# Performance work log

Measured on AMD Instinct MI355X. Metric: run time of the kernel, lower is better.

Reference implementation:

```python
import jax, jax.numpy as jnp
import numpy as np
from jax import lax

IN_PLANES = 64
OUT_PLANES = 128
NSAMPLE = 16
BN_EPS = 1e-5


def setup_inputs() -> dict:
    key = jax.random.key(0)
    k1, k2, k3 = jax.random.split(key, 3)
    B, N = 8, 8192
    xyz = jax.random.normal(k1, (B, N, 3), jnp.float32)
    feature = jax.random.normal(k2, (B, N, IN_PLANES), jnp.float32)
    W = jax.random.normal(k3, (OUT_PLANES, IN_PLANES), jnp.float32) * (1.0 / np.sqrt(IN_PLANES))
    gamma = jnp.ones((OUT_PLANES,), jnp.float32)
    beta = jnp.zeros((OUT_PLANES,), jnp.float32)
    return {"xyz": xyz, "feature": feature, "W": W, "gamma": gamma, "beta": beta, "npoint": 2048}


def farthest_point_sample(xyz, npoint):
    # xyz: [B, N, 3] -> centroids: [B, npoint] int32. Deterministic start at index 0
    # (torch version uses a random start; math is otherwise identical).
    B, N, _ = xyz.shape

    def step(carry, _):
        distance, farthest = carry  # [B,N], [B]
        centroid = jnp.take_along_axis(xyz, farthest[:, None, None], axis=1)  # [B,1,3]
        dist = jnp.sum((xyz - centroid) ** 2, axis=-1)  # [B,N]
        distance = jnp.minimum(distance, dist)
        new_far = jnp.argmax(distance, axis=-1).astype(jnp.int32)
        return (distance, new_far), farthest

    init = (jnp.full((B, N), 1e10, xyz.dtype), jnp.zeros((B,), jnp.int32))
    _, cents = lax.scan(step, init, None, length=npoint)  # [npoint, B]
    return cents.T  # [B, npoint]


def knn_point(nsample, xyz, new_xyz):
    # squared pairwise distances [B, M, N], then k smallest
    d = (-2.0 * jnp.einsum('bmc,bnc->bmn', new_xyz, xyz)
         + jnp.sum(new_xyz ** 2, -1)[:, :, None]
         + jnp.sum(xyz ** 2, -1)[:, None, :])
    _, idx = lax.top_k(-d, nsample)  # [B, M, nsample]
    return idx


def _forward(xyz, feature, W, gamma, beta, npoint):
    cent_idx = farthest_point_sample(xyz, npoint)  # [B, npoint]
    new_xyz = jnp.take_along_axis(xyz, cent_idx[:, :, None], axis=1)  # [B, npoint, 3]
    idx = knn_point(NSAMPLE, xyz, new_xyz)  # [B, npoint, K]
    grouped = jax.vmap(lambda f, i: f[i])(feature, idx)  # [B, npoint, K, Cin]
    h = jnp.einsum('bnkc,oc->bnko', grouped, W)  # Linear, bias=False
    # BatchNorm1d over flattened (B*npoint*K, Cout): per-channel batch stats
    m = jnp.mean(h, axis=(0, 1, 2))
    v = jnp.mean((h - m) ** 2, axis=(0, 1, 2))  # biased variance (torch normalization)
    h = (h - m) * lax.rsqrt(v + BN_EPS) * gamma + beta
    h = jax.nn.relu(h)
    new_feature = jnp.max(h, axis=2)  # max-pool over K neighbors
    return new_xyz, new_feature


def reference(xyz, feature, W, gamma, beta, npoint):
    return _forward(xyz, feature, W, gamma, beta, npoint)
```

## Files before the change

### kernel.cpp

```cpp
#include <hip/hip_runtime.h>
#include <stdint.h>

#define NPTS 8192
#define NBATCH 8
#define NPOINT 2048
#define KNN_K 16
#define CIN 64
#define COUT 128

typedef unsigned long long u64;
typedef unsigned int u32;

#define MAXU64(a, b) (((a) > (b)) ? (a) : (b))
#define MAXF64(a, b) fmax((a), (b))

__device__ __forceinline__ double wave_max_f64(double v) {
#define DPPSTEP(C)                                                             \
  {                                                                            \
    u64 k = (u64)__double_as_longlong(v);                                      \
    u32 lo = (u32)k, hi = (u32)(k >> 32);                                      \
    u32 nlo = (u32)__builtin_amdgcn_update_dpp(0, (int)lo, C, 0xf, 0xf, true); \
    u32 nhi = (u32)__builtin_amdgcn_update_dpp(0, (int)hi, C, 0xf, 0xf, true); \
    double o = __longlong_as_double((long long)(((u64)nhi << 32) | nlo));      \
    v = fmax(v, o);                                                            \
  }
  DPPSTEP(0x111)
  DPPSTEP(0x112)
  DPPSTEP(0x114)
  DPPSTEP(0x118)
  DPPSTEP(0x142)
  DPPSTEP(0x143)
#undef DPPSTEP
  return v;
}

__device__ __forceinline__ double row8_max_f64(double v) {
#define DPPSTEP(C)                                                             \
  {                                                                            \
    u64 k = (u64)__double_as_longlong(v);                                      \
    u32 lo = (u32)k, hi = (u32)(k >> 32);                                      \
    u32 nlo = (u32)__builtin_amdgcn_update_dpp(0, (int)lo, C, 0xf, 0xf, true); \
    u32 nhi = (u32)__builtin_amdgcn_update_dpp(0, (int)hi, C, 0xf, 0xf, true); \
    double o = __longlong_as_double((long long)(((u64)nhi << 32) | nlo));      \
    v = fmax(v, o);                                                            \
  }
  DPPSTEP(0x111)
  DPPSTEP(0x112)
  DPPSTEP(0x114)
#undef DPPSTEP
  return v;
}

__device__ __forceinline__ u64 wave_max_u64(u64 k) {
  u32 lo = (u32)k, hi = (u32)(k >> 32);
#define DPPSTEP(C)                                                             \
  {                                                                            \
    u32 nlo = (u32)__builtin_amdgcn_update_dpp(0, (int)lo, C, 0xf, 0xf, true); \
    u32 nhi = (u32)__builtin_amdgcn_update_dpp(0, (int)hi, C, 0xf, 0xf, true); \
    u64 cur = ((u64)hi << 32) | lo;                                            \
    u64 oth = ((u64)nhi << 32) | nlo;                                          \
    if (oth > cur) { hi = nhi; lo = nlo; }                                     \
  }
  DPPSTEP(0x111)
  DPPSTEP(0x112)
  DPPSTEP(0x114)
  DPPSTEP(0x118)
  DPPSTEP(0x142)
  DPPSTEP(0x143)
#undef DPPSTEP
  return ((u64)hi << 32) | lo;
}

__device__ __forceinline__ float wave_min_f32(float v) {
#define STEP(C)                                                                \
  {                                                                            \
    int o = __builtin_amdgcn_update_dpp((int)__float_as_uint(v),               \
                                        (int)__float_as_uint(v), C, 0xf, 0xf,  \
                                        false);                                \
    v = fminf(v, __uint_as_float((u32)o));                                     \
  }
  STEP(0x111) STEP(0x112) STEP(0x114) STEP(0x118) STEP(0x142) STEP(0x143)
#undef STEP
  return v;
}
__device__ __forceinline__ float wave_max_f32(float v) {
#define STEP(C)                                                                \
  {                                                                            \
    int o = __builtin_amdgcn_update_dpp((int)__float_as_uint(v),               \
                                        (int)__float_as_uint(v), C, 0xf, 0xf,  \
                                        false);                                \
    v = fmaxf(v, __uint_as_float((u32)o));                                     \
  }
  STEP(0x111) STEP(0x112) STEP(0x114) STEP(0x118) STEP(0x142) STEP(0x143)
#undef STEP
  return v;
}

__device__ __forceinline__ float bcast63(float v) {
  return __uint_as_float(
      (u32)__builtin_amdgcn_readlane((int)__float_as_uint(v), 63));
}

__device__ __forceinline__ u32 sp2(u32 v) {
  return (v & 1u) | ((v & 2u) << 2);
}

__global__ __launch_bounds__(512) void fps_kernel(const float* __restrict__ xyz,
                                                  int* __restrict__ cent) {
  const int b = blockIdx.x;
  const int tid = threadIdx.x;
  const int lane = tid & 63;
  const int wid = tid >> 6;
  const float* xb = xyz + (size_t)b * NPTS * 3;

  __shared__ __align__(16) float4 XYZ4[NPTS];
  __shared__ float gred[8][6];
  __shared__ int cnt64[64], base64[64], cur64[64];
  __shared__ __align__(16) double kbuf[2][8];

  float lx[16], ly[16], lz[16];
  float xl = 3e38f, xh = -3e38f, yl = 3e38f, yh = -3e38f, zl = 3e38f, zh = -3e38f;
#pragma unroll
  for (int j = 0; j < 16; ++j) {
    int i = tid + 512 * j;
    float x = xb[i * 3 + 0], y = xb[i * 3 + 1], z = xb[i * 3 + 2];
    lx[j] = x; ly[j] = y; lz[j] = z;
    xl = fminf(xl, x); xh = fmaxf(xh, x);
    yl = fminf(yl, y); yh = fmaxf(yh, y);
    zl = fminf(zl, z); zh = fmaxf(zh, z);
  }
  xl = wave_min_f32(xl); xh = wave_max_f32(xh);
  yl = wave_min_f32(yl); yh = wave_max_f32(yh);
  zl = wave_min_f32(zl); zh = wave_max_f32(zh);
  if (lane == 63) {
    gred[wid][0] = xl; gred[wid][1] = xh; gred[wid][2] = yl;
    gred[wid][3] = yh; gred[wid][4] = zl; gred[wid][5] = zh;
  }
  if (tid < 64) { cnt64[tid] = 0; cur64[tid] = 0; }
  __syncthreads();
  float gx0 = gred[0][0], gx1 = gred[0][1], gy0 = gred[0][2];
  float gy1 = gred[0][3], gz0 = gred[0][4], gz1 = gred[0][5];
#pragma unroll
  for (int w = 1; w < 8; ++w) {
    gx0 = fminf(gx0, gred[w][0]); gx1 = fmaxf(gx1, gred[w][1]);
    gy0 = fminf(gy0, gred[w][2]); gy1 = fmaxf(gy1, gred[w][3]);
    gz0 = fminf(gz0, gred[w][4]); gz1 = fmaxf(gz1, gred[w][5]);
  }
  const float sx = 4.f / fmaxf((gx1 - gx0) * 1.0001f, 1e-20f);
  const float sy = 4.f / fmaxf((gy1 - gy0) * 1.0001f, 1e-20f);
  const float sz = 4.f / fmaxf((gz1 - gz0) * 1.0001f, 1e-20f);

  int bin[16];
#pragma unroll
  for (int j = 0; j < 16; ++j) {
    u32 qx = (u32)min(3, max(0, (int)((lx[j] - gx0) * sx)));
    u32 qy = (u32)min(3, max(0, (int)((ly[j] - gy0) * sy)));
    u32 qz = (u32)min(3, max(0, (int)((lz[j] - gz0) * sz)));
    bin[j] = (int)((sp2(qx) << 2) | (sp2(qy) << 1) | sp2(qz));
    atomicAdd(&cnt64[bin[j]], 1);
  }
  __syncthreads();
  if (tid == 0) {
    int s = 0;
#pragma unroll
    for (int k = 0; k < 64; ++k) { base64[k] = s; s += cnt64[k]; }
  }
  __syncthreads();
#pragma unroll
  for (int j = 0; j < 16; ++j) {
    int i = tid + 512 * j;
    int pos = base64[bin[j]] + atomicAdd(&cur64[bin[j]], 1);
    XYZ4[pos] = make_float4(lx[j], ly[j], lz[j], __uint_as_float((u32)i));
  }
  if (tid == 0) cent[b * NPOINT] = 0;
  __syncthreads();

  float px[16], py[16], pz[16], dist[16];
  u32 klo[16];
  float axl = 3e38f, axh = -3e38f, ayl = 3e38f, ayh = -3e38f, azl = 3e38f, azh = -3e38f;
#pragma unroll
  for (int j = 0; j < 16; ++j) {
    int p = wid * 1024 + lane + 64 * j;
    float4 v = XYZ4[p];
    px[j] = v.x; py[j] = v.y; pz[j] = v.z;
    dist[j] = 1e10f;
    klo[j] = ((8191u - __float_as_uint(v.w)) << 13) | (u32)p;
    axl = fminf(axl, v.x); axh = fmaxf(axh, v.x);
    ayl = fminf(ayl, v.y); ayh = fmaxf(ayh, v.y);
    azl = fminf(azl, v.z); azh = fmaxf(azh, v.z);
  }
  const float bx0 = bcast63(wave_min_f32(axl)), bx1 = bcast63(wave_max_f32(axh));
  const float by0 = bcast63(wave_min_f32(ayl)), by1 = bcast63(wave_max_f32(ayh));
  const float bz0 = bcast63(wave_min_f32(azl)), bz1 = bcast63(wave_max_f32(azh));

  float cx = xb[0], cy = xb[1], cz = xb[2];
  float dmax = 1e10f;
  double prev_wk = 0.0;

  for (int it = 1; it < NPOINT; ++it) {
    float ax = fmaxf(fmaxf(bx0 - cx, cx - bx1), 0.f);
    float ay = fmaxf(fmaxf(by0 - cy, cy - by1), 0.f);
    float az = fmaxf(fmaxf(bz0 - cz, cz - bz1), 0.f);
    float LB = ax * ax + ay * ay + az * az;
    int skip = (LB > dmax * 1.00002f) ? 1 : 0;
    skip = __builtin_amdgcn_readfirstlane(skip);
    double wk;
    if (skip) {
      wk = prev_wk;
    } else {
      double key[16];
#pragma unroll
      for (int j = 0; j < 16; ++j) {
        float dx = px[j] - cx, dy = py[j] - cy, dz = pz[j] - cz;
        float dd = dx * dx + dy * dy + dz * dz;
        float t = fminf(dist[j], dd);
        dist[j] = t;
        key[j] = __longlong_as_double(
            (long long)(((u64)__float_as_uint(t) << 32) | klo[j]));
      }
#pragma unroll
      for (int s = 1; s < 16; s <<= 1) {
#pragma unroll
        for (int j = 0; j < 16; j += 2 * s) key[j] = MAXF64(key[j], key[j + s]);
      }
      wk = wave_max_f64(key[0]);
      prev_wk = wk;
      dmax = __uint_as_float((u32)__builtin_amdgcn_readlane(
          (int)(u32)(((u64)__double_as_longlong(wk)) >> 32), 63));
    }
    if (lane == 63) kbuf[it & 1][wid] = wk;
    __syncthreads();
    double kv = kbuf[it & 1][lane & 7];
    kv = row8_max_f64(kv);
    u32 rlo = (u32)__builtin_amdgcn_readlane(
        (int)(u32)(u64)__double_as_longlong(kv), 7);
    u32 pos = rlo & 8191u;
    if (tid == 0) cent[b * NPOINT + it] = (int)(8191u - ((rlo >> 13) & 8191u));
    float4 c4 = XYZ4[pos];
    cx = c4.x; cy = c4.y; cz = c4.z;
  }
}

__global__ __launch_bounds__(256) void knn_kernel(const float* __restrict__ xyz,
                                                  const int* __restrict__ cent,
                                                  int* __restrict__ knn,
                                                  float* __restrict__ out_xyz) {
  const int pt = blockIdx.x;
  const int b = pt >> 11;
  const int tid = threadIdx.x;
  const float* xb = xyz + (size_t)b * NPTS * 3;
  const int ci = cent[pt];
  const float mx = xb[ci * 3 + 0], my = xb[ci * 3 + 1], mz = xb[ci * 3 + 2];
  if (tid < 3) out_xyz[pt * 3 + tid] = xb[ci * 3 + tid];
  const float sm = mx * mx + my * my + mz * mz;

  float d[32];
  float lv = 3.0e38f;
  int lj = 0;
#pragma unroll
  for (int j = 0; j < 32; ++j) {
    int i = tid + 256 * j;
    float x = xb[i * 3 + 0], y = xb[i * 3 + 1], z = xb[i * 3 + 2];
    float dot = mx * x + my * y + mz * z;
    float sp = x * x + y * y + z * z;
    float dd = -2.0f * dot + sm + sp;
    d[j] = dd;
    if (dd < lv) { lv = dd; lj = j; }
  }

  __shared__ __align__(16) u64 kbuf[2][4];
  const int lane = tid & 63;

  for (int p = 0; p < KNN_K; ++p) {
    u32 fb = __float_as_uint(lv);
    u32 mapped = (fb & 0x80000000u) ? ~fb : (fb | 0x80000000u);
    u32 idx = (u32)(tid + (lj << 8));
    u64 ik = ~(((u64)mapped << 32) | (u64)idx);
    u64 wk = wave_max_u64(ik);
    if (lane == 63) kbuf[p & 1][tid >> 6] = wk;
    __syncthreads();
    const ulonglong2* kb = (const ulonglong2*)&kbuf[p & 1][0];
    ulonglong2 q0 = kb[0], q1 = kb[1];
    u64 best = MAXU64(MAXU64(q0.x, q0.y), MAXU64(q1.x, q1.y));
    u32 widx = (u32)(~best);
    if (tid == 0) knn[pt * KNN_K + p] = (int)widx;
    if (tid == (int)(widx & 255u)) {
      int j0 = (int)(widx >> 8);
      float nlv = 3.0e38f;
      int nlj = 0;
#pragma unroll
      for (int j = 0; j < 32; ++j) {
        if (j == j0) d[j] = 3.0e38f;
        if (d[j] < nlv) { nlv = d[j]; nlj = j; }
      }
      lv = nlv; lj = nlj;
    }
  }
}

__global__ __launch_bounds__(256) void gemm_stats_kernel(const float* __restrict__ feat,
                                                         const float* __restrict__ W,
                                                         const int* __restrict__ knn,
                                                         float* __restrict__ part,
                                                         float* __restrict__ mxbuf,
                                                         float* __restrict__ mnbuf) {
  const int tid = threadIdx.x;
  const int o0 = (tid & 63) * 2;
  const int o1 = o0 + 1;
  const int grp = tid >> 6;
  __shared__ __align__(16) float g[128][CIN];
  __shared__ int kidx[128];
  __shared__ float sred[4][128];

  const int rowbase = blockIdx.x * 128;
  if (tid < 128) kidx[tid] = knn[rowbase + tid];

  float4 w0v[16], w1v[16];
  {
    const float4* wv0 = (const float4*)(W + (size_t)o0 * CIN);
    const float4* wv1 = (const float4*)(W + (size_t)o1 * CIN);
#pragma unroll
    for (int q = 0; q < 16; ++q) { w0v[q] = wv0[q]; w1v[q] = wv1[q]; }
  }
  __syncthreads();
#pragma unroll
  for (int s = 0; s < 8; ++s) {
    int v = tid + 256 * s;
    int row = v >> 4, q = v & 15;
    int gr = rowbase + row;
    int bb = gr >> 15;
    const float4* src = (const float4*)(feat + (size_t)(bb * NPTS + kidx[row]) * CIN);
    *((float4*)&g[row][q * 4]) = src[q];
  }
  __syncthreads();

  float s1_0 = 0.f, s2_0 = 0.f, s1_1 = 0.f, s2_1 = 0.f;
#pragma unroll
  for (int pp = 0; pp < 2; ++pp) {
    const int ptl = grp + pp * 4;
    float mx0 = -3.0e38f, mn0 = 3.0e38f, mx1 = -3.0e38f, mn1 = 3.0e38f;
#pragma unroll
    for (int k = 0; k < KNN_K; ++k) {
      const int row = ptl * 16 + k;
      float a0 = 0.f, a1 = 0.f;
#pragma unroll
      for (int q = 0; q < 16; ++q) {
        float4 a = *((const float4*)&g[row][q * 4]);
        a0 += w0v[q].x * a.x + w0v[q].y * a.y + w0v[q].z * a.z + w0v[q].w * a.w;
        a1 += w1v[q].x * a.x + w1v[q].y * a.y + w1v[q].z * a.z + w1v[q].w * a.w;
      }
      s1_0 += a0; s2_0 += a0 * a0; mx0 = fmaxf(mx0, a0); mn0 = fminf(mn0, a0);
      s1_1 += a1; s2_1 += a1 * a1; mx1 = fmaxf(mx1, a1); mn1 = fminf(mn1, a1);
    }
    const size_t pt = (size_t)blockIdx.x * 8 + ptl;
    mxbuf[pt * COUT + o0] = mx0;
    mxbuf[pt * COUT + o1] = mx1;
    mnbuf[pt * COUT + o0] = mn0;
    mnbuf[pt * COUT + o1] = mn1;
  }
  sred[grp][o0] = s1_0; sred[grp][o1] = s1_1;
  __syncthreads();
  if (tid < 128) {
    float t = sred[0][tid] + sred[1][tid] + sred[2][tid] + sred[3][tid];
    part[blockIdx.x * 256 + tid] = t;
  }
  __syncthreads();
  sred[grp][o0] = s2_0; sred[grp][o1] = s2_1;
  __syncthreads();
  if (tid < 128) {
    float t = sred[0][tid] + sred[1][tid] + sred[2][tid] + sred[3][tid];
    part[blockIdx.x * 256 + 128 + tid] = t;
  }
}

__global__ __launch_bounds__(256) void bn_reduce_kernel(const float* __restrict__ part,
                                                        const float* __restrict__ gamma,
                                                        const float* __restrict__ beta,
                                                        float* __restrict__ stats) {
  const int o = blockIdx.x;
  const int tid = threadIdx.x;
  float s1 = 0.f, s2 = 0.f;
  for (int p = tid; p < 2048; p += 256) {
    s1 += part[p * 256 + o];
    s2 += part[p * 256 + 128 + o];
  }
  __shared__ float r1[256], r2[256];
  r1[tid] = s1; r2[tid] = s2;
  __syncthreads();
  for (int s = 128; s >= 1; s >>= 1) {
    if (tid < s) { r1[tid] += r1[tid + s]; r2[tid] += r2[tid + s]; }
    __syncthreads();
  }
  if (tid == 0) {
    const float n = (float)(NBATCH * NPOINT * KNN_K);
    float mean = r1[0] / n;
    float var = r2[0] / n - mean * mean;
    float inv = rsqrtf(var + 1e-5f);
    float sc = gamma[o] * inv;
    stats[o] = sc;
    stats[128 + o] = beta[o] - mean * sc;
  }
}

__global__ __launch_bounds__(256) void finalize_kernel(float* __restrict__ out_feat,
                                                       const float* __restrict__ mnbuf,
                                                       const float* __restrict__ stats) {
  const int i = blockIdx.x * 256 + threadIdx.x;
  const int o = i & 127;
  const float sc = stats[o];
  const float sh = stats[128 + o];
  const float mx = out_feat[i];
  const float mn = mnbuf[i];
  const float sel = (sc >= 0.f) ? mx : mn;
  out_feat[i] = fmaxf(sel * sc + sh, 0.f);
}

extern "C" void kernel_launch(void* const* d_in, const int* in_sizes, int n_in,
                              void* d_out, int out_size, void* d_ws, size_t ws_size,
                              hipStream_t stream) {
  const float* xyz = (const float*)d_in[0];
  const float* feat = (const float*)d_in[1];
  const float* W = (const float*)d_in[2];
  const float* gamma = (const float*)d_in[3];
  const float* beta = (const float*)d_in[4];
  float* out = (float*)d_out;

  int* cent = (int*)d_ws;
  int* knn = cent + NBATCH * NPOINT;
  float* part = (float*)(knn + NBATCH * NPOINT * KNN_K);
  float* stats = part + 2048 * 256;
  float* mnbuf = stats + 256;

  float* out_xyz = out;
  float* out_feat = out + NBATCH * NPOINT * 3;

  hipLaunchKernelGGL(fps_kernel, dim3(NBATCH), dim3(512), 0, stream, xyz, cent);
  hipLaunchKernelGGL(knn_kernel, dim3(NBATCH * NPOINT), dim3(256), 0, stream,
                     xyz, cent, knn, out_xyz);
  hipLaunchKernelGGL(gemm_stats_kernel, dim3(2048), dim3(256), 0, stream,
                     feat, W, knn, part, out_feat, mnbuf);
  hipLaunchKernelGGL(bn_reduce_kernel, dim3(128), dim3(256), 0, stream,
                     part, gamma, beta, stats);
  hipLaunchKernelGGL(finalize_kernel, dim3(8192), dim3(256), 0, stream,
                     out_feat, mnbuf, stats);
}
```

Measured before the change: 1.998 ms.

## Speculatively pick two FPS centroids per barrier using top-2 wave reduction

Each wave now reduces both its largest and second-largest distance keys, and the block-level reduction picks the global top-2. If the second candidate's distance is unchanged after applying the first centroid, both are emitted in one iteration and the next distance update folds in two centroids. This aims to roughly halve the number of block-wide barriers and serial iterations in farthest-point sampling. The cost is extra reduction work per iteration and a second DPP pass, with a correctness subtlety around ties.

```diff
diff --git a/kernel.cpp b/kernel.cpp
--- a/kernel.cpp
+++ b/kernel.cpp
@@ -34,7 +34,7 @@
   return v;
 }
 
-__device__ __forceinline__ double row8_max_f64(double v) {
+__device__ __forceinline__ double row16_max_f64(double v) {
 #define DPPSTEP(C)                                                             \
   {                                                                            \
     u64 k = (u64)__double_as_longlong(v);                                      \
@@ -47,6 +47,7 @@
   DPPSTEP(0x111)
   DPPSTEP(0x112)
   DPPSTEP(0x114)
+  DPPSTEP(0x118)
 #undef DPPSTEP
   return v;
 }
@@ -116,7 +117,7 @@
   __shared__ __align__(16) float4 XYZ4[NPTS];
   __shared__ float gred[8][6];
   __shared__ int cnt64[64], base64[64], cur64[64];
-  __shared__ __align__(16) double kbuf[2][8];
+  __shared__ __align__(16) u64 kbuf[2][16];
 
   float lx[16], ly[16], lz[16];
   float xl = 3e38f, xh = -3e38f, yl = 3e38f, yh = -3e38f, zl = 3e38f, zh = -3e38f;
@@ -193,51 +194,120 @@
   const float by0 = bcast63(wave_min_f32(ayl)), by1 = bcast63(wave_max_f32(ayh));
   const float bz0 = bcast63(wave_min_f32(azl)), bz1 = bcast63(wave_max_f32(azh));
 
-  float cx = xb[0], cy = xb[1], cz = xb[2];
+  float c1x = xb[0], c1y = xb[1], c1z = xb[2];
+  float c2x = 0.f, c2y = 0.f, c2z = 0.f;
+  int has2 = 0;
+  u64 m1w = 0, m2w = 0;
   float dmax = 1e10f;
-  double prev_wk = 0.0;
-
-  for (int it = 1; it < NPOINT; ++it) {
-    float ax = fmaxf(fmaxf(bx0 - cx, cx - bx1), 0.f);
-    float ay = fmaxf(fmaxf(by0 - cy, cy - by1), 0.f);
-    float az = fmaxf(fmaxf(bz0 - cz, cz - bz1), 0.f);
-    float LB = ax * ax + ay * ay + az * az;
-    int skip = (LB > dmax * 1.00002f) ? 1 : 0;
-    skip = __builtin_amdgcn_readfirstlane(skip);
-    double wk;
-    if (skip) {
-      wk = prev_wk;
-    } else {
+  int rp = 0;
+  int it = 1;
+
+  while (it < NPOINT) {
+    float ax = fmaxf(fmaxf(bx0 - c1x, c1x - bx1), 0.f);
+    float ay = fmaxf(fmaxf(by0 - c1y, c1y - by1), 0.f);
+    float az = fmaxf(fmaxf(bz0 - c1z, c1z - bz1), 0.f);
+    float LB1 = ax * ax + ay * ay + az * az;
+    int dirty = (LB1 <= dmax * 1.00002f) ? 1 : 0;
+    if (has2) {
+      float bx = fmaxf(fmaxf(bx0 - c2x, c2x - bx1), 0.f);
+      float by = fmaxf(fmaxf(by0 - c2y, c2y - by1), 0.f);
+      float bz = fmaxf(fmaxf(bz0 - c2z, c2z - bz1), 0.f);
+      float LB2 = bx * bx + by * by + bz * bz;
+      dirty |= (LB2 <= dmax * 1.00002f) ? 1 : 0;
+    }
+    dirty = __builtin_amdgcn_readfirstlane(dirty);
+
+    if (dirty) {
+      if (has2) {
+#pragma unroll
+        for (int j = 0; j < 16; ++j) {
+          float dx = px[j] - c1x, dy = py[j] - c1y, dz = pz[j] - c1z;
+          float dd = dx * dx + dy * dy + dz * dz;
+          float ex = px[j] - c2x, ey = py[j] - c2y, ez = pz[j] - c2z;
+          float ee = ex * ex + ey * ey + ez * ez;
+          dist[j] = fminf(fminf(dist[j], dd), ee);
+        }
+      } else {
+#pragma unroll
+        for (int j = 0; j < 16; ++j) {
+          float dx = px[j] - c1x, dy = py[j] - c1y, dz = pz[j] - c1z;
+          float dd = dx * dx + dy * dy + dz * dz;
+          dist[j] = fminf(dist[j], dd);
+        }
+      }
       double key[16];
 #pragma unroll
-      for (int j = 0; j < 16; ++j) {
-        float dx = px[j] - cx, dy = py[j] - cy, dz = pz[j] - cz;
-        float dd = dx * dx + dy * dy + dz * dz;
-        float t = fminf(dist[j], dd);
-        dist[j] = t;
+      for (int j = 0; j < 16; ++j)
         key[j] = __longlong_as_double(
-            (long long)(((u64)__float_as_uint(t) << 32) | klo[j]));
-      }
+            (long long)(((u64)__float_as_uint(dist[j]) << 32) | klo[j]));
 #pragma unroll
       for (int s = 1; s < 16; s <<= 1) {
 #pragma unroll
         for (int j = 0; j < 16; j += 2 * s) key[j] = MAXF64(key[j], key[j + s]);
       }
-      wk = wave_max_f64(key[0]);
-      prev_wk = wk;
-      dmax = __uint_as_float((u32)__builtin_amdgcn_readlane(
-          (int)(u32)(((u64)__double_as_longlong(wk)) >> 32), 63));
+      double wk = wave_max_f64(key[0]);
+      u64 wkb = (u64)__double_as_longlong(wk);
+      u32 m1lo_ = (u32)__builtin_amdgcn_readlane((int)(u32)wkb, 63);
+      u32 m1hi_ = (u32)__builtin_amdgcn_readlane((int)(u32)(wkb >> 32), 63);
+      m1w = ((u64)m1hi_ << 32) | m1lo_;
+      dmax = __uint_as_float(m1hi_);
+      double r2 = 0.0;
+#pragma unroll
+      for (int j = 0; j < 16; ++j) {
+        double kj = __longlong_as_double(
+            (long long)(((u64)__float_as_uint(dist[j]) << 32) | klo[j]));
+        kj = (klo[j] == m1lo_) ? 0.0 : kj;
+        r2 = MAXF64(r2, kj);
+      }
+      double wk2 = wave_max_f64(r2);
+      u64 wk2b = (u64)__double_as_longlong(wk2);
+      u32 m2lo_ = (u32)__builtin_amdgcn_readlane((int)(u32)wk2b, 63);
+      u32 m2hi_ = (u32)__builtin_amdgcn_readlane((int)(u32)(wk2b >> 32), 63);
+      m2w = ((u64)m2hi_ << 32) | m2lo_;
     }
-    if (lane == 63) kbuf[it & 1][wid] = wk;
+    if (lane == 63) {
+      kbuf[rp][wid] = m1w;
+      kbuf[rp][8 + wid] = m2w;
+    }
     __syncthreads();
-    double kv = kbuf[it & 1][lane & 7];
-    kv = row8_max_f64(kv);
-    u32 rlo = (u32)__builtin_amdgcn_readlane(
-        (int)(u32)(u64)__double_as_longlong(kv), 7);
-    u32 pos = rlo & 8191u;
-    if (tid == 0) cent[b * NPOINT + it] = (int)(8191u - ((rlo >> 13) & 8191u));
-    float4 c4 = XYZ4[pos];
-    cx = c4.x; cy = c4.y; cz = c4.z;
+
+    u64 kv = kbuf[rp][lane & 15];
+    double kd = __longlong_as_double((long long)kv);
+    double kr = row16_max_f64(kd);
+    u64 krb = (u64)__double_as_longlong(kr);
+    u32 g1lo = (u32)__builtin_amdgcn_readlane((int)(u32)krb, 15);
+    u32 g1hi = (u32)__builtin_amdgcn_readlane((int)(u32)(krb >> 32), 15);
+    u64 g1 = ((u64)g1hi << 32) | g1lo;
+    double kd2 = (kv == g1) ? 0.0 : kd;
+    double kr2 = row16_max_f64(kd2);
+    u64 kr2b = (u64)__double_as_longlong(kr2);
+    u32 g2lo = (u32)__builtin_amdgcn_readlane((int)(u32)kr2b, 15);
+    u32 g2hi = (u32)__builtin_amdgcn_readlane((int)(u32)(kr2b >> 32), 15);
+
+    u32 pos1 = g1lo & 8191u;
+    u32 pos2 = g2lo & 8191u;
+    float4 cc1 = XYZ4[pos1];
+    float4 cc2 = XYZ4[pos2];
+    if (tid == 0) cent[b * NPOINT + it] = (int)(8191u - ((g1lo >> 13) & 8191u));
+
+    float qdx = cc2.x - cc1.x, qdy = cc2.y - cc1.y, qdz = cc2.z - cc1.z;
+    float qdd = qdx * qdx + qdy * qdy + qdz * qdz;
+    float qdist = __uint_as_float(g2hi);
+    float tq = fminf(qdist, qdd);
+    int hit = (__float_as_uint(tq) == g2hi) && (it + 1 < NPOINT);
+
+    c1x = cc1.x; c1y = cc1.y; c1z = cc1.z;
+    if (hit) {
+      if (tid == 0)
+        cent[b * NPOINT + it + 1] = (int)(8191u - ((g2lo >> 13) & 8191u));
+      c2x = cc2.x; c2y = cc2.y; c2z = cc2.z;
+      has2 = 1;
+      it += 2;
+    } else {
+      has2 = 0;
+      it += 1;
+    }
+    rp ^= 1;
   }
 }
 
```

Result: slower. 2.243 ms (+12.2%).

## Compute per-wave top-16 in KNN then merge once, removing per-step block syncs

Applied to the files above, without the earlier changes.

The KNN kernel now gives each wave a contiguous 2048-point slice. Each wave independently extracts its own 16 nearest candidates and writes them to shared memory. One wave then merges the 4x16 candidates with 16 wave-max reductions. This replaces 16 block-wide __syncthreads and shared-memory exchanges with a single barrier. The cost is extra selection work per wave (16 picks in every wave instead of one global pick) and a serial merge step in wave 0.

```diff
diff --git a/kernel.cpp b/kernel.cpp
--- a/kernel.cpp
+++ b/kernel.cpp
@@ -248,6 +248,8 @@
   const int pt = blockIdx.x;
   const int b = pt >> 11;
   const int tid = threadIdx.x;
+  const int lane = tid & 63;
+  const int wid = tid >> 6;
   const float* xb = xyz + (size_t)b * NPTS * 3;
   const int ci = cent[pt];
   const float mx = xb[ci * 3 + 0], my = xb[ci * 3 + 1], mz = xb[ci * 3 + 2];
@@ -259,7 +261,7 @@
   int lj = 0;
 #pragma unroll
   for (int j = 0; j < 32; ++j) {
-    int i = tid + 256 * j;
+    int i = wid * 2048 + lane + 64 * j;
     float x = xb[i * 3 + 0], y = xb[i * 3 + 1], z = xb[i * 3 + 2];
     float dot = mx * x + my * y + mz * z;
     float sp = x * x + y * y + z * z;
@@ -268,24 +270,20 @@
     if (dd < lv) { lv = dd; lj = j; }
   }
 
-  __shared__ __align__(16) u64 kbuf[2][4];
-  const int lane = tid & 63;
+  __shared__ __align__(16) u64 kw[4][KNN_K];
 
   for (int p = 0; p < KNN_K; ++p) {
     u32 fb = __float_as_uint(lv);
     u32 mapped = (fb & 0x80000000u) ? ~fb : (fb | 0x80000000u);
-    u32 idx = (u32)(tid + (lj << 8));
+    u32 idx = (u32)(wid * 2048 + lane + (lj << 6));
     u64 ik = ~(((u64)mapped << 32) | (u64)idx);
     u64 wk = wave_max_u64(ik);
-    if (lane == 63) kbuf[p & 1][tid >> 6] = wk;
-    __syncthreads();
-    const ulonglong2* kb = (const ulonglong2*)&kbuf[p & 1][0];
-    ulonglong2 q0 = kb[0], q1 = kb[1];
-    u64 best = MAXU64(MAXU64(q0.x, q0.y), MAXU64(q1.x, q1.y));
-    u32 widx = (u32)(~best);
-    if (tid == 0) knn[pt * KNN_K + p] = (int)widx;
-    if (tid == (int)(widx & 255u)) {
-      int j0 = (int)(widx >> 8);
+    u32 wlo = (u32)__builtin_amdgcn_readlane((int)(u32)wk, 63);
+    u32 whi = (u32)__builtin_amdgcn_readlane((int)(u32)(wk >> 32), 63);
+    if (lane == 63) kw[wid][p] = ((u64)whi << 32) | wlo;
+    u32 widx = ~wlo;
+    if (lane == (int)(widx & 63u)) {
+      int j0 = (int)((widx >> 6) & 31u);
       float nlv = 3.0e38f;
       int nlj = 0;
 #pragma unroll
@@ -294,6 +292,18 @@
         if (d[j] < nlv) { nlv = d[j]; nlj = j; }
       }
       lv = nlv; lj = nlj;
+    }
+  }
+  __syncthreads();
+
+  if (wid == 0) {
+    u64 k = kw[lane >> 4][lane & 15];
+    for (int p = 0; p < KNN_K; ++p) {
+      u64 m = wave_max_u64(k);
+      u32 mlo = (u32)__builtin_amdgcn_readlane((int)(u32)m, 63);
+      u32 mhi = (u32)__builtin_amdgcn_readlane((int)(u32)(m >> 32), 63);
+      if (lane == 0) knn[pt * KNN_K + p] = (int)(~mlo);
+      if (k == (((u64)mhi << 32) | mlo)) k = 0;
     }
   }
 }
```

Result: no change. 2.028 ms (+1.5%).
